# Kernel tuning notes

Measured on AMD Instinct MI355X. Metric: run time of the kernel, lower is better.

The kernel has to match this reference:

```python
import jax, jax.numpy as jnp
import numpy as np

T_TOTAL = 90  # t_total init arg (static decode length)


def _gru_cell(x, h, w_ih, w_hh, b_ih, b_hh):
    # PyTorch nn.GRUCell math
    gi = x @ w_ih.T + b_ih
    gh = h @ w_hh.T + b_hh
    i_r, i_z, i_n = jnp.split(gi, 3, axis=-1)
    h_r, h_z, h_n = jnp.split(gh, 3, axis=-1)
    r = jax.nn.sigmoid(i_r + h_r)
    z = jax.nn.sigmoid(i_z + h_z)
    n = jnp.tanh(i_n + r * h_n)
    return (1.0 - z) * n + z * h


def setup_inputs() -> dict:
    key = jax.random.key(0)
    T, B, NX, H, NZ = 90, 2048, 144, 128, 128
    M1, M2 = 300, 200
    ks = jax.random.split(key, 24)
    def p(k, shape):
        return jax.random.normal(k, shape, dtype=jnp.float32) * 0.05
    return {
        "x": jax.random.normal(ks[0], (T, B, NX), dtype=jnp.float32),
        # encoder GRUCell (nx -> H)
        "w_ih_e": p(ks[1], (3 * H, NX)), "w_hh_e": p(ks[2], (3 * H, H)),
        "b_ih_e": p(ks[3], (3 * H,)),   "b_hh_e": p(ks[4], (3 * H,)),
        # encoder MLP (tanh) H->300->200
        "W1e": p(ks[5], (M1, H)),  "b1e": p(ks[6], (M1,)),
        "W2e": p(ks[7], (M2, M1)), "b2e": p(ks[8], (M2,)),
        # latent heads 200->NZ
        "Wmu": p(ks[9], (NZ, M2)),  "bmu": p(ks[10], (NZ,)),
        "Wlv": p(ks[11], (NZ, M2)), "blv": p(ks[12], (NZ,)),
        # decoder GRUCell (nx+nz -> H)
        "w_ih_d": p(ks[13], (3 * H, NX + NZ)), "w_hh_d": p(ks[14], (3 * H, H)),
        "b_ih_d": p(ks[15], (3 * H,)),          "b_hh_d": p(ks[16], (3 * H,)),
        # decoder MLP (tanh) H->300->200 and output 200->nx
        "W1d": p(ks[17], (M1, H)),  "b1d": p(ks[18], (M1,)),
        "W2d": p(ks[19], (M2, M1)), "b2d": p(ks[20], (M2,)),
        "Wo": p(ks[21], (NX, M2)),  "bo": p(ks[22], (NX,)),
    }


def reference(x, w_ih_e, w_hh_e, b_ih_e, b_hh_e, W1e, b1e, W2e, b2e,
              Wmu, bmu, Wlv, blv, w_ih_d, w_hh_d, b_ih_d, b_hh_d,
              W1d, b1d, W2d, b2d, Wo, bo):
    B = x.shape[1]
    H = w_hh_e.shape[1]
    h0 = jnp.zeros((B, H), dtype=x.dtype)

    # ---- encode: GRU over time, take last hidden ----
    def enc_step(h, xt):
        return _gru_cell(xt, h, w_ih_e, w_hh_e, b_ih_e, b_hh_e), None
    h_x, _ = jax.lax.scan(enc_step, h0, x)  # (B, H)
    he = jnp.tanh(h_x @ W1e.T + b1e)
    he = jnp.tanh(he @ W2e.T + b2e)
    mu = he @ Wmu.T + bmu
    logvar = he @ Wlv.T + blv
    z = mu  # eval mode: z = mu (no reparameterization noise)

    def dec_step(carry, _):
        hd, xp = carry
        rnn_in = jnp.concatenate([xp, z], axis=1)  # (B, NX+NZ)
        hd = _gru_cell(rnn_in, hd, w_ih_d, w_hh_d, b_ih_d, b_hh_d)
        m = jnp.tanh(hd @ W1d.T + b1d)
        m = jnp.tanh(m @ W2d.T + b2d)
        xi = m @ Wo.T + bo
        return (hd, xi), xi

    _, x_rec = jax.lax.scan(dec_step, (h0, x[0]), None, length=T_TOTAL)
    return x_rec, mu, logvar
```

## Files before the change

### kernel.cpp

```cpp
#include <hip/hip_runtime.h>
#include <cstddef>

#define T_STEPS 90
#define BT      2048
#define NXV     144
#define HV      128
#define NZV     128
#define M1V     300
#define M2V     200
#define NB      16
#define NTH     512

typedef __attribute__((ext_vector_type(8))) _Float16 half8v;
typedef __attribute__((ext_vector_type(4))) float f32x4;

constexpr int MTa[12]   = {24,24,19,13, 8, 8,24,24,24,19,13, 9};
constexpr int MREAL[12] = {384,384,300,200,128,128,384,384,384,300,200,144};
constexpr int KREAL[12] = {144,128,128,300,200,200,144,128,128,128,300,200};
constexpr int RSW[12]   = {144,128,128,300,200,200,272,272,128,128,300,200};
constexpr int COW[12]   = {  0,  0,  0,  0,  0,  0,  0,144,  0,  0,  0,  0};
constexpr int P13[13]   = {0,120,240,335,465,521,577,697,817,937,1032,1162,1225};
constexpr int NFRAG = 1225;

__device__ __forceinline__ float fsig(float v)  { return 1.0f / (1.0f + __expf(-v)); }
__device__ __forceinline__ float ftanh(float v) { return 1.0f - 2.0f / (__expf(2.0f * v) + 1.0f); }

__global__ void __launch_bounds__(64)
prep_frags(const float* __restrict__ w_ih_e, const float* __restrict__ w_hh_e,
           const float* __restrict__ W1e,    const float* __restrict__ W2e,
           const float* __restrict__ Wmu,    const float* __restrict__ Wlv,
           const float* __restrict__ w_ih_d, const float* __restrict__ w_hh_d,
           const float* __restrict__ W1d,    const float* __restrict__ W2d,
           const float* __restrict__ Wo,
           const float* __restrict__ b_ih_e, const float* __restrict__ b_hh_e,
           const float* __restrict__ b1e,    const float* __restrict__ b2e,
           const float* __restrict__ bmu,    const float* __restrict__ blv,
           const float* __restrict__ b_ih_d, const float* __restrict__ b_hh_d,
           const float* __restrict__ b1d,    const float* __restrict__ b2d,
           const float* __restrict__ bo,
           _Float16* __restrict__ ws)
{
    int f = blockIdx.x;
    int g = 0;
    while (g < 11 && f >= P13[g + 1]) ++g;
    int fl = f - P13[g];
    int MT = MTa[g];
    int kt = fl / MT, mt = fl - kt * MT;

    const float* W; const float* bias;
    switch (g) {
        case 0:  W = w_ih_e; bias = b_ih_e; break;
        case 1:  W = w_hh_e; bias = b_hh_e; break;
        case 2:  W = W1e;    bias = b1e;    break;
        case 3:  W = W2e;    bias = b2e;    break;
        case 4:  W = Wmu;    bias = bmu;    break;
        case 5:  W = Wlv;    bias = blv;    break;
        case 6:  W = w_ih_d; bias = nullptr; break;
        case 7:  W = w_ih_d; bias = b_ih_d; break;
        case 8:  W = w_hh_d; bias = b_hh_d; break;
        case 9:  W = W1d;    bias = b1d;    break;
        case 10: W = W2d;    bias = b2d;    break;
        default: W = Wo;     bias = bo;     break;
    }
    int l = threadIdx.x;
    int m  = mt * 16 + (l & 15);
    int kb = kt * 32 + (l >> 4) * 8;
    _Float16* dst = ws + (size_t)f * 512 + (size_t)l * 8;
    #pragma unroll
    for (int j = 0; j < 8; ++j) {
        int k = kb + j;
        float val = 0.0f;
        if (m < MREAL[g]) {
            if (k < KREAL[g]) val = W[(size_t)m * RSW[g] + COW[g] + k];
            else if (k == KREAL[g] && bias) val = bias[m];
        }
        dst[j] = (_Float16)val;
    }
}

template<int MT, int KT, int NT, int RS>
__device__ __forceinline__ void gemm_reg(const half8v (&af)[KT * NT],
                                         const _Float16* __restrict__ Bt,
                                         int w, int l, f32x4 (&acc)[NT])
{
    const int bo_ = (l & 15) * RS + ((l >> 4) << 3);
    #pragma unroll
    for (int kt = 0; kt < KT; ++kt) {
        half8v bf = *(const half8v*)(Bt + bo_ + kt * 32);
        #pragma unroll
        for (int i = 0; i < NT; ++i)
            if (w + 8 * i < MT)
                acc[i] = __builtin_amdgcn_mfma_f32_16x16x32_f16(af[kt * NT + i], bf, acc[i], 0, 0, 0);
    }
}

template<int MT, int KT, int NT, int RS>
__device__ __forceinline__ void mlp_stream(const half8v* __restrict__ A,
                                           const _Float16* __restrict__ Bt,
                                           int w, int l, f32x4 (&acc)[NT])
{
    half8v af[NT * KT];
    #pragma unroll
    for (int i = 0; i < NT; ++i) {
        int mt = w + 8 * i;
        if (mt < MT) {
            #pragma unroll
            for (int kt = 0; kt < KT; ++kt)
                af[i * KT + kt] = A[(size_t)(kt * MT + mt) * 64 + l];
        }
    }
    const int bo_ = (l & 15) * RS + ((l >> 4) << 3);
    #pragma unroll
    for (int kt = 0; kt < KT; ++kt) {
        half8v bf = *(const half8v*)(Bt + bo_ + kt * 32);
        #pragma unroll
        for (int i = 0; i < NT; ++i) {
            int mt = w + 8 * i;
            if (mt < MT)
                acc[i] = __builtin_amdgcn_mfma_f32_16x16x32_f16(af[i * KT + kt], bf, acc[i], 0, 0, 0);
        }
    }
}

template<int MT, int KT, int NT, int RS>
__device__ __forceinline__ void mlp_lds(const _Float16* __restrict__ Alds,
                                        const _Float16* __restrict__ Bt,
                                        int w, int l, f32x4 (&acc)[NT])
{
    const int bo_ = (l & 15) * RS + ((l >> 4) << 3);
    #pragma unroll
    for (int kt = 0; kt < KT; ++kt) {
        half8v bf = *(const half8v*)(Bt + bo_ + kt * 32);
        #pragma unroll
        for (int i = 0; i < NT; ++i) {
            int mt = w + 8 * i;
            if (mt < MT) {
                half8v af = *(const half8v*)(Alds + ((size_t)(kt * MT + mt) * 64 + l) * 8);
                acc[i] = __builtin_amdgcn_mfma_f32_16x16x32_f16(af, bf, acc[i], 0, 0, 0);
            }
        }
    }
}

template<int MT, int NT, int RS>
__device__ __forceinline__ void write_tanhN(const f32x4 (&acc)[NT], int Mreal,
                                            _Float16* __restrict__ T, int w, int l)
{
    int b = l & 15, q4 = (l >> 4) << 2;
    #pragma unroll
    for (int i = 0; i < NT; ++i) {
        int mt = w + 8 * i;
        if (mt < MT) {
            #pragma unroll
            for (int r = 0; r < 4; ++r) {
                int m = mt * 16 + q4 + r;
                if (m < Mreal) T[b * RS + m] = (_Float16)ftanh(acc[i][r]);
            }
        }
    }
}

__global__ void __launch_bounds__(NTH, 2)
vae_mfma(const float* __restrict__ x, const half8v* __restrict__ wsv,
         float* __restrict__ out)
{
    __shared__ __align__(16) _Float16 xT [NB * 168];
    __shared__ __align__(16) _Float16 hT [NB * 168];
    __shared__ __align__(16) _Float16 m1T[NB * 328];
    __shared__ __align__(16) _Float16 m2T[NB * 232];
    __shared__ __align__(16) _Float16 g10L[130 * 512];

    const int tid = threadIdx.x;
    const int w = tid >> 6, l = tid & 63;
    const int bbase = blockIdx.x * NB;
    const size_t XREC_SZ = (size_t)T_STEPS * BT * NXV;
    const size_t MU_OFF = XREC_SZ;
    const size_t LV_OFF = XREC_SZ + (size_t)BT * NZV;
    const f32x4 z4 = {0.f, 0.f, 0.f, 0.f};

#define AHI(g) (wsv + (size_t)P13[g] * 64)

    auto load_x = [&](int t, float xr[5]) {
        #pragma unroll
        for (int u = 0; u < 5; ++u) {
            int i = u * NTH + tid;
            if (i < NB * NXV)
                xr[u] = __builtin_nontemporal_load(
                    &x[(size_t)t * (BT * NXV) + (size_t)(bbase + i / NXV) * NXV + (i % NXV)]);
        }
    };
    auto store_x = [&](const float xr[5]) {
        #pragma unroll
        for (int u = 0; u < 5; ++u) {
            int i = u * NTH + tid;
            if (i < NB * NXV) {
                int b2 = i / NXV, k = i - b2 * NXV;
                xT[b2 * 168 + k] = (_Float16)xr[u];
            }
        }
    };

    half8v gih[15], ghh[15];
    half8v w1df[15];
    auto load_gates = [&](const half8v* Gih, const half8v* Ghh) {
        #pragma unroll
        for (int kt = 0; kt < 5; ++kt) {
            #pragma unroll
            for (int j = 0; j < 3; ++j) {
                gih[kt * 3 + j] = Gih[(size_t)(kt * 24 + w + 8 * j) * 64 + l];
                ghh[kt * 3 + j] = Ghh[(size_t)(kt * 24 + w + 8 * j) * 64 + l];
            }
        }
    };

    float hreg[4] = {0.f, 0.f, 0.f, 0.f};
    auto gru_combine = [&](const f32x4 (&ai)[3], const f32x4 (&ah)[3]) {
        #pragma unroll
        for (int r = 0; r < 4; ++r) {
            float rr = fsig(ai[0][r] + ah[0][r]);
            float zz = fsig(ai[1][r] + ah[1][r]);
            float nn = ftanh(ai[2][r] + rr * ah[2][r]);
            hreg[r] = (1.f - zz) * nn + zz * hreg[r];
        }
    };
    auto write_h = [&]() {
        int jb = 16 * w + ((l >> 4) << 2), b = l & 15;
        #pragma unroll
        for (int r = 0; r < 4; ++r) hT[b * 168 + jb + r] = (_Float16)hreg[r];
    };

    for (int i = tid; i < NB * 168; i += NTH) { xT[i] = (_Float16)0.f; hT[i] = (_Float16)0.f; }
    for (int i = tid; i < NB * 328; i += NTH) m1T[i] = (_Float16)0.f;
    for (int i = tid; i < NB * 232; i += NTH) m2T[i] = (_Float16)0.f;
    for (int i = tid; i < 130 * 64; i += NTH)
        *(half8v*)(g10L + (size_t)i * 8) = AHI(10)[i];
    load_gates(AHI(0), AHI(1));
    float xr[5] = {0, 0, 0, 0, 0};
    load_x(0, xr);
    __syncthreads();
    if (tid < NB) {
        xT [tid * 168 + 144] = (_Float16)1.f;
        hT [tid * 168 + 128] = (_Float16)1.f;
        m1T[tid * 328 + 300] = (_Float16)1.f;
        m2T[tid * 232 + 200] = (_Float16)1.f;
    }
    store_x(xr);
    load_x(1, xr);
    __syncthreads();

    for (int t = 0; t < T_STEPS; ++t) {
        f32x4 ai[3] = {z4, z4, z4}, ah[3] = {z4, z4, z4};
        gemm_reg<24, 5, 3, 168>(gih, xT, w, l, ai);
        gemm_reg<24, 5, 3, 168>(ghh, hT, w, l, ah);
        gru_combine(ai, ah);
        __syncthreads();
        write_h();
        if (t + 1 < T_STEPS) {
            store_x(xr);
            if (t + 2 < T_STEPS) load_x(t + 2, xr);
        }
        __syncthreads();
    }

    {
        f32x4 a1[3] = {z4, z4, z4};
        mlp_stream<19, 5, 3, 168>(AHI(2), hT, w, l, a1);
        write_tanhN<19, 3, 328>(a1, M1V, m1T, w, l);
        __syncthreads();
        f32x4 a2[2] = {z4, z4};
        mlp_stream<13, 10, 2, 328>(AHI(3), m1T, w, l, a2);
        write_tanhN<13, 2, 232>(a2, M2V, m2T, w, l);
        __syncthreads();
        f32x4 am[1] = {z4}, av[1] = {z4};
        mlp_stream<8, 7, 1, 232>(AHI(4), m2T, w, l, am);
        mlp_stream<8, 7, 1, 232>(AHI(5), m2T, w, l, av);
        __syncthreads();
        int b = l & 15, q4 = (l >> 4) << 2;
        int m = w * 16 + q4;
        __builtin_nontemporal_store(am[0], (f32x4*)&out[MU_OFF + (size_t)(bbase + b) * NZV + m]);
        __builtin_nontemporal_store(av[0], (f32x4*)&out[LV_OFF + (size_t)(bbase + b) * NZV + m]);
        #pragma unroll
        for (int r = 0; r < 4; ++r)
            m1T[b * 328 + m + r] = (_Float16)am[0][r];
    }

    f32x4 gzr[3] = {z4, z4, z4};
    {
        for (int i = tid; i < NB * HV; i += NTH) {
            int b2 = i >> 7, j = i & 127;
            hT[b2 * 168 + j] = (_Float16)0.f;
        }
        if (tid < NB) m1T[tid * 328 + 128] = (_Float16)1.f;
        float xr0[5] = {0, 0, 0, 0, 0};
        load_x(0, xr0);
        store_x(xr0);
        __syncthreads();
        mlp_stream<24, 5, 3, 328>(AHI(7), m1T, w, l, gzr);
        load_gates(AHI(6), AHI(8));
        #pragma unroll
        for (int kt = 0; kt < 5; ++kt) {
            #pragma unroll
            for (int j = 0; j < 3; ++j)
                if (w + 8 * j < 19)
                    w1df[kt * 3 + j] = AHI(9)[(size_t)(kt * 19 + w + 8 * j) * 64 + l];
        }
        #pragma unroll
        for (int r = 0; r < 4; ++r) hreg[r] = 0.f;
    }
    __syncthreads();

    for (int t = 0; t < T_STEPS; ++t) {
        f32x4 ai[3], ah[3];
        #pragma unroll
        for (int i = 0; i < 3; ++i) { ai[i] = gzr[i]; ah[i] = z4; }
        gemm_reg<24, 5, 3, 168>(gih, xT, w, l, ai);
        gemm_reg<24, 5, 3, 168>(ghh, hT, w, l, ah);
        gru_combine(ai, ah);
        __syncthreads();
        write_h();
        __syncthreads();
        f32x4 a1[3] = {z4, z4, z4};
        gemm_reg<19, 5, 3, 168>(w1df, hT, w, l, a1);
        write_tanhN<19, 3, 328>(a1, M1V, m1T, w, l);
        __syncthreads();
        half8v wo_af[14];
        #pragma unroll
        for (int kt = 0; kt < 7; ++kt) {
            #pragma unroll
            for (int i = 0; i < 2; ++i)
                if (w + 8 * i < 9)
                    wo_af[kt * 2 + i] = AHI(11)[(size_t)(kt * 9 + w + 8 * i) * 64 + l];
        }
        f32x4 a2[2] = {z4, z4};
        mlp_lds<13, 10, 2, 328>(g10L, m1T, w, l, a2);
        write_tanhN<13, 2, 232>(a2, M2V, m2T, w, l);
        __syncthreads();
        f32x4 ao[2] = {z4, z4};
        gemm_reg<9, 7, 2, 232>(wo_af, m2T, w, l, ao);
        {
            int b = l & 15, q4 = (l >> 4) << 2;
            #pragma unroll
            for (int i2 = 0; i2 < 2; ++i2) {
                int mt = w + 8 * i2;
                if (mt < 9) {
                    int m = mt * 16 + q4;
                    __builtin_nontemporal_store(ao[i2],
                        (f32x4*)&out[(size_t)t * (BT * NXV) + (size_t)(bbase + b) * NXV + m]);
                    #pragma unroll
                    for (int r = 0; r < 4; ++r)
                        xT[b * 168 + m + r] = (_Float16)ao[i2][r];
                }
            }
        }
        __syncthreads();
    }
#undef AHI
}

extern "C" void kernel_launch(void* const* d_in, const int* in_sizes, int n_in,
                              void* d_out, int out_size, void* d_ws, size_t ws_size,
                              hipStream_t stream) {
    (void)in_sizes; (void)n_in; (void)out_size; (void)ws_size;
    const float* p[23];
    for (int i = 0; i < 23; ++i) p[i] = (const float*)d_in[i];
    _Float16* ws = (_Float16*)d_ws;

    prep_frags<<<dim3(NFRAG), dim3(64), 0, stream>>>(
        p[1], p[2], p[5], p[7], p[9], p[11], p[13], p[14], p[17], p[19], p[21],
        p[3], p[4], p[6], p[8], p[10], p[12], p[15], p[16], p[18], p[20], p[22],
        ws);

    vae_mfma<<<dim3(BT / NB), dim3(NTH), 0, stream>>>(
        p[0], (const half8v*)ws, (float*)d_out);
}
```

Baseline: 912.5 us.

## Move biases to register epilogues, double-buffer hidden state, split W2d between LDS and registers

Biases are no longer folded into the weight fragments as an extra K column. They are held in registers and added in the GRU combine and tanh epilogues, with vectorized half4 LDS writes. The hidden-state and input LDS tiles are double-buffered, which removes one __syncthreads per encoder and decoder step. The decoder's second MLP layer keeps the first six K-tiles in LDS and the last four in registers, shrinking the LDS footprint. Register pressure rises (w2df, wo14, bias arrays), and dropping the bias column can shorten some K loops.

```diff
diff --git a/kernel.cpp b/kernel.cpp
--- a/kernel.cpp
+++ b/kernel.cpp
@@ -12,6 +12,7 @@
 #define NTH     512
 
 typedef __attribute__((ext_vector_type(8))) _Float16 half8v;
+typedef __attribute__((ext_vector_type(4))) _Float16 half4v;
 typedef __attribute__((ext_vector_type(4))) float f32x4;
 
 constexpr int MTa[12]   = {24,24,19,13, 8, 8,24,24,24,19,13, 9};
@@ -32,12 +33,6 @@
            const float* __restrict__ w_ih_d, const float* __restrict__ w_hh_d,
            const float* __restrict__ W1d,    const float* __restrict__ W2d,
            const float* __restrict__ Wo,
-           const float* __restrict__ b_ih_e, const float* __restrict__ b_hh_e,
-           const float* __restrict__ b1e,    const float* __restrict__ b2e,
-           const float* __restrict__ bmu,    const float* __restrict__ blv,
-           const float* __restrict__ b_ih_d, const float* __restrict__ b_hh_d,
-           const float* __restrict__ b1d,    const float* __restrict__ b2d,
-           const float* __restrict__ bo,
            _Float16* __restrict__ ws)
 {
     int f = blockIdx.x;
@@ -46,21 +41,14 @@
     int fl = f - P13[g];
     int MT = MTa[g];
     int kt = fl / MT, mt = fl - kt * MT;
-
-    const float* W; const float* bias;
+    const float* W;
     switch (g) {
-        case 0:  W = w_ih_e; bias = b_ih_e; break;
-        case 1:  W = w_hh_e; bias = b_hh_e; break;
-        case 2:  W = W1e;    bias = b1e;    break;
-        case 3:  W = W2e;    bias = b2e;    break;
-        case 4:  W = Wmu;    bias = bmu;    break;
-        case 5:  W = Wlv;    bias = blv;    break;
-        case 6:  W = w_ih_d; bias = nullptr; break;
-        case 7:  W = w_ih_d; bias = b_ih_d; break;
-        case 8:  W = w_hh_d; bias = b_hh_d; break;
-        case 9:  W = W1d;    bias = b1d;    break;
-        case 10: W = W2d;    bias = b2d;    break;
-        default: W = Wo;     bias = bo;     break;
+        case 0:  W = w_ih_e; break;  case 1:  W = w_hh_e; break;
+        case 2:  W = W1e;    break;  case 3:  W = W2e;    break;
+        case 4:  W = Wmu;    break;  case 5:  W = Wlv;    break;
+        case 6:  W = w_ih_d; break;  case 7:  W = w_ih_d; break;
+        case 8:  W = w_hh_d; break;  case 9:  W = W1d;    break;
+        case 10: W = W2d;    break;  default: W = Wo;     break;
     }
     int l = threadIdx.x;
     int m  = mt * 16 + (l & 15);
@@ -69,17 +57,14 @@
     #pragma unroll
     for (int j = 0; j < 8; ++j) {
         int k = kb + j;
-        float val = 0.0f;
-        if (m < MREAL[g]) {
-            if (k < KREAL[g]) val = W[(size_t)m * RSW[g] + COW[g] + k];
-            else if (k == KREAL[g] && bias) val = bias[m];
-        }
+        float val = (m < MREAL[g] && k < KREAL[g])
+                  ? W[(size_t)m * RSW[g] + COW[g] + k] : 0.0f;
         dst[j] = (_Float16)val;
     }
 }
 
 template<int MT, int KT, int NT, int RS>
-__device__ __forceinline__ void gemm_reg(const half8v (&af)[KT * NT],
+__device__ __forceinline__ void gemm_reg(const half8v* af,
                                          const _Float16* __restrict__ Bt,
                                          int w, int l, f32x4 (&acc)[NT])
 {
@@ -114,36 +99,14 @@
     for (int kt = 0; kt < KT; ++kt) {
         half8v bf = *(const half8v*)(Bt + bo_ + kt * 32);
         #pragma unroll
-        for (int i = 0; i < NT; ++i) {
-            int mt = w + 8 * i;
-            if (mt < MT)
+        for (int i = 0; i < NT; ++i)
+            if (w + 8 * i < MT)
                 acc[i] = __builtin_amdgcn_mfma_f32_16x16x32_f16(af[i * KT + kt], bf, acc[i], 0, 0, 0);
-        }
-    }
-}
-
-template<int MT, int KT, int NT, int RS>
-__device__ __forceinline__ void mlp_lds(const _Float16* __restrict__ Alds,
-                                        const _Float16* __restrict__ Bt,
-                                        int w, int l, f32x4 (&acc)[NT])
-{
-    const int bo_ = (l & 15) * RS + ((l >> 4) << 3);
-    #pragma unroll
-    for (int kt = 0; kt < KT; ++kt) {
-        half8v bf = *(const half8v*)(Bt + bo_ + kt * 32);
-        #pragma unroll
-        for (int i = 0; i < NT; ++i) {
-            int mt = w + 8 * i;
-            if (mt < MT) {
-                half8v af = *(const half8v*)(Alds + ((size_t)(kt * MT + mt) * 64 + l) * 8);
-                acc[i] = __builtin_amdgcn_mfma_f32_16x16x32_f16(af, bf, acc[i], 0, 0, 0);
-            }
-        }
     }
 }
 
 template<int MT, int NT, int RS>
-__device__ __forceinline__ void write_tanhN(const f32x4 (&acc)[NT], int Mreal,
+__device__ __forceinline__ void write_tanhV(const f32x4 (&acc)[NT], const float* bias,
                                             _Float16* __restrict__ T, int w, int l)
 {
     int b = l & 15, q4 = (l >> 4) << 2;
@@ -151,27 +114,35 @@
     for (int i = 0; i < NT; ++i) {
         int mt = w + 8 * i;
         if (mt < MT) {
-            #pragma unroll
-            for (int r = 0; r < 4; ++r) {
-                int m = mt * 16 + q4 + r;
-                if (m < Mreal) T[b * RS + m] = (_Float16)ftanh(acc[i][r]);
-            }
+            half4v v;
+            #pragma unroll
+            for (int r = 0; r < 4; ++r) v[r] = (_Float16)ftanh(acc[i][r] + bias[i * 4 + r]);
+            *(half4v*)&T[b * RS + mt * 16 + q4] = v;
         }
     }
 }
 
 __global__ void __launch_bounds__(NTH, 2)
 vae_mfma(const float* __restrict__ x, const half8v* __restrict__ wsv,
+         const float* __restrict__ b_ih_e, const float* __restrict__ b_hh_e,
+         const float* __restrict__ b1e,    const float* __restrict__ b2e,
+         const float* __restrict__ bmu,    const float* __restrict__ blv,
+         const float* __restrict__ b_ih_d, const float* __restrict__ b_hh_d,
+         const float* __restrict__ b1d,    const float* __restrict__ b2d,
+         const float* __restrict__ bo,
          float* __restrict__ out)
 {
-    __shared__ __align__(16) _Float16 xT [NB * 168];
-    __shared__ __align__(16) _Float16 hT [NB * 168];
+    __shared__ __align__(16) _Float16 xT [2][NB * 168];
+    __shared__ __align__(16) _Float16 hT [2][NB * 168];
     __shared__ __align__(16) _Float16 m1T[NB * 328];
     __shared__ __align__(16) _Float16 m2T[NB * 232];
-    __shared__ __align__(16) _Float16 g10L[130 * 512];
+    __shared__ __align__(16) _Float16 g10L[78 * 512];
 
     const int tid = threadIdx.x;
     const int w = tid >> 6, l = tid & 63;
+    const int b_ = l & 15;
+    const int q4 = (l >> 4) << 2;
+    const int u  = w * 16 + q4;
     const int bbase = blockIdx.x * NB;
     const size_t XREC_SZ = (size_t)T_STEPS * BT * NXV;
     const size_t MU_OFF = XREC_SZ;
@@ -182,81 +153,101 @@
 
     auto load_x = [&](int t, float xr[5]) {
         #pragma unroll
-        for (int u = 0; u < 5; ++u) {
-            int i = u * NTH + tid;
+        for (int uu = 0; uu < 5; ++uu) {
+            int i = uu * NTH + tid;
             if (i < NB * NXV)
-                xr[u] = __builtin_nontemporal_load(
+                xr[uu] = __builtin_nontemporal_load(
                     &x[(size_t)t * (BT * NXV) + (size_t)(bbase + i / NXV) * NXV + (i % NXV)]);
         }
     };
-    auto store_x = [&](const float xr[5]) {
-        #pragma unroll
-        for (int u = 0; u < 5; ++u) {
-            int i = u * NTH + tid;
+    auto store_x = [&](_Float16* dst, const float xr[5]) {
+        #pragma unroll
+        for (int uu = 0; uu < 5; ++uu) {
+            int i = uu * NTH + tid;
             if (i < NB * NXV) {
                 int b2 = i / NXV, k = i - b2 * NXV;
-                xT[b2 * 168 + k] = (_Float16)xr[u];
-            }
-        }
-    };
-
-    half8v gih[15], ghh[15];
-    half8v w1df[15];
+                dst[b2 * 168 + k] = (_Float16)xr[uu];
+            }
+        }
+    };
+
+    half8v gih[15] = {}, ghh[15] = {};
     auto load_gates = [&](const half8v* Gih, const half8v* Ghh) {
         #pragma unroll
-        for (int kt = 0; kt < 5; ++kt) {
+        for (int kt = 0; kt < 5; ++kt)
             #pragma unroll
             for (int j = 0; j < 3; ++j) {
                 gih[kt * 3 + j] = Gih[(size_t)(kt * 24 + w + 8 * j) * 64 + l];
                 ghh[kt * 3 + j] = Ghh[(size_t)(kt * 24 + w + 8 * j) * 64 + l];
             }
-        }
     };
 
     float hreg[4] = {0.f, 0.f, 0.f, 0.f};
+    float gb[16];
     auto gru_combine = [&](const f32x4 (&ai)[3], const f32x4 (&ah)[3]) {
         #pragma unroll
         for (int r = 0; r < 4; ++r) {
-            float rr = fsig(ai[0][r] + ah[0][r]);
-            float zz = fsig(ai[1][r] + ah[1][r]);
-            float nn = ftanh(ai[2][r] + rr * ah[2][r]);
+            float rr = fsig(ai[0][r] + ah[0][r] + gb[r]);
+            float zz = fsig(ai[1][r] + ah[1][r] + gb[4 + r]);
+            float nn = ftanh(ai[2][r] + gb[8 + r] + rr * (ah[2][r] + gb[12 + r]));
             hreg[r] = (1.f - zz) * nn + zz * hreg[r];
         }
     };
-    auto write_h = [&]() {
-        int jb = 16 * w + ((l >> 4) << 2), b = l & 15;
-        #pragma unroll
-        for (int r = 0; r < 4; ++r) hT[b * 168 + jb + r] = (_Float16)hreg[r];
-    };
-
-    for (int i = tid; i < NB * 168; i += NTH) { xT[i] = (_Float16)0.f; hT[i] = (_Float16)0.f; }
+    auto write_h = [&](int p) {
+        half4v v;
+        #pragma unroll
+        for (int r = 0; r < 4; ++r) v[r] = (_Float16)hreg[r];
+        *(half4v*)&hT[p][b_ * 168 + u] = v;
+    };
+
+    float b1r[12], b2r[8];
+    auto load_mlp_bias = [&](const float* B1, const float* B2) {
+        #pragma unroll
+        for (int i = 0; i < 3; ++i)
+            #pragma unroll
+            for (int r = 0; r < 4; ++r) {
+                int m = (w + 8 * i) * 16 + q4 + r;
+                b1r[i * 4 + r] = B1[m < M1V ? m : M1V - 1];
+            }
+        #pragma unroll
+        for (int i = 0; i < 2; ++i)
+            #pragma unroll
+            for (int r = 0; r < 4; ++r) {
+                int m = (w + 8 * i) * 16 + q4 + r;
+                b2r[i * 4 + r] = B2[m < M2V ? m : M2V - 1];
+            }
+    };
+
+    for (int i = tid; i < 2 * NB * 168; i += NTH) { ((_Float16*)xT)[i] = (_Float16)0.f; ((_Float16*)hT)[i] = (_Float16)0.f; }
     for (int i = tid; i < NB * 328; i += NTH) m1T[i] = (_Float16)0.f;
     for (int i = tid; i < NB * 232; i += NTH) m2T[i] = (_Float16)0.f;
-    for (int i = tid; i < 130 * 64; i += NTH)
+    for (int i = tid; i < 78 * 64; i += NTH)
         *(half8v*)(g10L + (size_t)i * 8) = AHI(10)[i];
     load_gates(AHI(0), AHI(1));
+    #pragma unroll
+    for (int r = 0; r < 4; ++r) {
+        gb[r]      = b_ih_e[u + r]       + b_hh_e[u + r];
+        gb[4 + r]  = b_ih_e[128 + u + r] + b_hh_e[128 + u + r];
+        gb[8 + r]  = b_ih_e[256 + u + r];
+        gb[12 + r] = b_hh_e[256 + u + r];
+    }
+    load_mlp_bias(b1e, b2e);
     float xr[5] = {0, 0, 0, 0, 0};
     load_x(0, xr);
     __syncthreads();
-    if (tid < NB) {
-        xT [tid * 168 + 144] = (_Float16)1.f;
-        hT [tid * 168 + 128] = (_Float16)1.f;
-        m1T[tid * 328 + 300] = (_Float16)1.f;
-        m2T[tid * 232 + 200] = (_Float16)1.f;
-    }
-    store_x(xr);
+    store_x(xT[0], xr);
     load_x(1, xr);
     __syncthreads();
 
     for (int t = 0; t < T_STEPS; ++t) {
+        int p = t & 1;
         f32x4 ai[3] = {z4, z4, z4}, ah[3] = {z4, z4, z4};
-        gemm_reg<24, 5, 3, 168>(gih, xT, w, l, ai);
-        gemm_reg<24, 5, 3, 168>(ghh, hT, w, l, ah);
+        gemm_reg<24, 5, 3, 168>(gih, xT[p], w, l, ai);
+        gemm_reg<24, 5, 3, 168>(ghh, hT[p], w, l, ah);
         gru_combine(ai, ah);
-        __syncthreads();
-        write_h();
+        write_h(p ^ 1);
         if (t + 1 < T_STEPS) {
-            store_x(xr);
+            store_x(xT[p ^ 1], xr);
             if (t + 2 < T_STEPS) load_x(t + 2, xr);
         }
         __syncthreads();
@@ -264,92 +255,135 @@
 
     {
         f32x4 a1[3] = {z4, z4, z4};
-        mlp_stream<19, 5, 3, 168>(AHI(2), hT, w, l, a1);
-        write_tanhN<19, 3, 328>(a1, M1V, m1T, w, l);
+        mlp_stream<19, 5, 3, 168>(AHI(2), hT[0], w, l, a1);
+        write_tanhV<19, 3, 328>(a1, b1r, m1T, w, l);
         __syncthreads();
         f32x4 a2[2] = {z4, z4};
         mlp_stream<13, 10, 2, 328>(AHI(3), m1T, w, l, a2);
-        write_tanhN<13, 2, 232>(a2, M2V, m2T, w, l);
+        write_tanhV<13, 2, 232>(a2, b2r, m2T, w, l);
         __syncthreads();
         f32x4 am[1] = {z4}, av[1] = {z4};
         mlp_stream<8, 7, 1, 232>(AHI(4), m2T, w, l, am);
         mlp_stream<8, 7, 1, 232>(AHI(5), m2T, w, l, av);
-        __syncthreads();
-        int b = l & 15, q4 = (l >> 4) << 2;
-        int m = w * 16 + q4;
-        __builtin_nontemporal_store(am[0], (f32x4*)&out[MU_OFF + (size_t)(bbase + b) * NZV + m]);
-        __builtin_nontemporal_store(av[0], (f32x4*)&out[LV_OFF + (size_t)(bbase + b) * NZV + m]);
-        #pragma unroll
-        for (int r = 0; r < 4; ++r)
-            m1T[b * 328 + m + r] = (_Float16)am[0][r];
-    }
+        f32x4 vm, vv;
+        half4v zv;
+        #pragma unroll
+        for (int r = 0; r < 4; ++r) {
+            vm[r] = am[0][r] + bmu[u + r];
+            vv[r] = av[0][r] + blv[u + r];
+            zv[r] = (_Float16)vm[r];
+        }
+        __builtin_nontemporal_store(vm, (f32x4*)&out[MU_OFF + (size_t)(bbase + b_) * NZV + u]);
+        __builtin_nontemporal_store(vv, (f32x4*)&out[LV_OFF + (size_t)(bbase + b_) * NZV + u]);
+        *(half4v*)&m1T[b_ * 328 + u] = zv;
+    }
+    __syncthreads();
 
     f32x4 gzr[3] = {z4, z4, z4};
+    half8v w1df[15] = {}, w2df[8] = {}, wo14[14] = {};
     {
-        for (int i = tid; i < NB * HV; i += NTH) {
-            int b2 = i >> 7, j = i & 127;
-            hT[b2 * 168 + j] = (_Float16)0.f;
-        }
-        if (tid < NB) m1T[tid * 328 + 128] = (_Float16)1.f;
+        for (int i = tid; i < NB * 168; i += NTH) hT[0][i] = (_Float16)0.f;
         float xr0[5] = {0, 0, 0, 0, 0};
         load_x(0, xr0);
-        store_x(xr0);
-        __syncthreads();
+        store_x(xT[0], xr0);
         mlp_stream<24, 5, 3, 328>(AHI(7), m1T, w, l, gzr);
+        #pragma unroll
+        for (int j = 0; j < 3; ++j)
+            #pragma unroll
+            for (int r = 0; r < 4; ++r) gzr[j][r] += b_ih_d[u + 128 * j + r];
         load_gates(AHI(6), AHI(8));
         #pragma unroll
-        for (int kt = 0; kt < 5; ++kt) {
+        for (int kt = 0; kt < 5; ++kt)
             #pragma unroll
             for (int j = 0; j < 3; ++j)
                 if (w + 8 * j < 19)
                     w1df[kt * 3 + j] = AHI(9)[(size_t)(kt * 19 + w + 8 * j) * 64 + l];
-        }
-        #pragma unroll
-        for (int r = 0; r < 4; ++r) hreg[r] = 0.f;
-    }
-    __syncthreads();
-
-    for (int t = 0; t < T_STEPS; ++t) {
-        f32x4 ai[3], ah[3];
-        #pragma unroll
-        for (int i = 0; i < 3; ++i) { ai[i] = gzr[i]; ah[i] = z4; }
-        gemm_reg<24, 5, 3, 168>(gih, xT, w, l, ai);
-        gemm_reg<24, 5, 3, 168>(ghh, hT, w, l, ah);
-        gru_combine(ai, ah);
-        __syncthreads();
-        write_h();
-        __syncthreads();
-        f32x4 a1[3] = {z4, z4, z4};
-        gemm_reg<19, 5, 3, 168>(w1df, hT, w, l, a1);
-        write_tanhN<19, 3, 328>(a1, M1V, m1T, w, l);
-        __syncthreads();
-        half8v wo_af[14];
-        #pragma unroll
-        for (int kt = 0; kt < 7; ++kt) {
+        #pragma unroll
+        for (int kt = 0; kt < 4; ++kt)
+            #pragma unroll
+            for (int i = 0; i < 2; ++i)
+                if (w + 8 * i < 13)
+                    w2df[kt * 2 + i] = AHI(10)[(size_t)((6 + kt) * 13 + w + 8 * i) * 64 + l];
+        #pragma unroll
+        for (int kt = 0; kt < 7; ++kt)
             #pragma unroll
             for (int i = 0; i < 2; ++i)
                 if (w + 8 * i < 9)
-                    wo_af[kt * 2 + i] = AHI(11)[(size_t)(kt * 9 + w + 8 * i) * 64 + l];
-        }
+                    wo14[kt * 2 + i] = AHI(11)[(size_t)(kt * 9 + w + 8 * i) * 64 + l];
+        #pragma unroll
+        for (int r = 0; r < 4; ++r) {
+            gb[r]      = b_hh_d[u + r];
+            gb[4 + r]  = b_hh_d[128 + u + r];
+            gb[8 + r]  = 0.f;
+            gb[12 + r] = b_hh_d[256 + u + r];
+            hreg[r] = 0.f;
+        }
+        load_mlp_bias(b1d, b2d);
+    }
+    float bor[8];
+    #pragma unroll
+    for (int i = 0; i < 2; ++i)
+        #pragma unroll
+        for (int r = 0; r < 4; ++r) {
+            int m = (w + 8 * i) * 16 + q4 + r;
+            bor[i * 4 + r] = bo[m < NXV ? m : NXV - 1];
+        }
+    __syncthreads();
+
+    for (int t = 0; t < T_STEPS; ++t) {
+        int q = t & 1;
+        f32x4 ai[3], ah[3];
+        #pragma unroll
+        for (int i = 0; i < 3; ++i) { ai[i] = gzr[i]; ah[i] = z4; }
+        gemm_reg<24, 5, 3, 168>(gih, xT[0], w, l, ai);
+        gemm_reg<24, 5, 3, 168>(ghh, hT[q], w, l, ah);
+        gru_combine(ai, ah);
+        write_h(q ^ 1);
+        __syncthreads();
+        f32x4 a1[3] = {z4, z4, z4};
+        gemm_reg<19, 5, 3, 168>(w1df, hT[q ^ 1], w, l, a1);
+        write_tanhV<19, 3, 328>(a1, b1r, m1T, w, l);
+        __syncthreads();
         f32x4 a2[2] = {z4, z4};
-        mlp_lds<13, 10, 2, 328>(g10L, m1T, w, l, a2);
-        write_tanhN<13, 2, 232>(a2, M2V, m2T, w, l);
+        {
+            const int bo2 = b_ * 328 + ((l >> 4) << 3);
+            #pragma unroll
+            for (int kt = 0; kt < 6; ++kt) {
+                half8v bf = *(const half8v*)(m1T + bo2 + kt * 32);
+                #pragma unroll
+                for (int i = 0; i < 2; ++i)
+                    if (w + 8 * i < 13) {
+                        half8v af = *(const half8v*)(g10L + ((size_t)(kt * 13 + w + 8 * i) * 64 + l) * 8);
+                        a2[i] = __builtin_amdgcn_mfma_f32_16x16x32_f16(af, bf, a2[i], 0, 0, 0);
+                    }
+            }
+            #pragma unroll
+            for (int kt = 0; kt < 4; ++kt) {
+                half8v bf = *(const half8v*)(m1T + bo2 + (6 + kt) * 32);
+                #pragma unroll
+                for (int i = 0; i < 2; ++i)
+                    if (w + 8 * i < 13)
+                        a2[i] = __builtin_amdgcn_mfma_f32_16x16x32_f16(w2df[kt * 2 + i], bf, a2[i], 0, 0, 0);
+            }
+        }
+        write_tanhV<13, 2, 232>(a2, b2r, m2T, w, l);
         __syncthreads();
         f32x4 ao[2] = {z4, z4};
-        gemm_reg<9, 7, 2, 232>(wo_af, m2T, w, l, ao);
-        {
-            int b = l & 15, q4 = (l >> 4) << 2;
-            #pragma unroll
-            for (int i2 = 0; i2 < 2; ++i2) {
-                int mt = w + 8 * i2;
-                if (mt < 9) {
-                    int m = mt * 16 + q4;
-                    __builtin_nontemporal_store(ao[i2],
-                        (f32x4*)&out[(size_t)t * (BT * NXV) + (size_t)(bbase + b) * NXV + m]);
-                    #pragma unroll
-                    for (int r = 0; r < 4; ++r)
-                        xT[b * 168 + m + r] = (_Float16)ao[i2][r];
+        gemm_reg<9, 7, 2, 232>(wo14, m2T, w, l, ao);
+        #pragma unroll
+        for (int i2 = 0; i2 < 2; ++i2) {
+            int mt = w + 8 * i2;
+            if (mt < 9) {
+                f32x4 vo;
+                half4v vh;
+                #pragma unroll
+                for (int r = 0; r < 4; ++r) {
+                    vo[r] = ao[i2][r] + bor[i2 * 4 + r];
+                    vh[r] = (_Float16)vo[r];
                 }
+                __builtin_nontemporal_store(vo,
+                    (f32x4*)&out[(size_t)t * (BT * NXV) + (size_t)(bbase + b_) * NXV + mt * 16 + q4]);
+                *(half4v*)&xT[0][b_ * 168 + mt * 16 + q4] = vh;
             }
         }
         __syncthreads();
@@ -366,10 +400,15 @@
     _Float16* ws = (_Float16*)d_ws;
 
     prep_frags<<<dim3(NFRAG), dim3(64), 0, stream>>>(
-        p[1], p[2], p[5], p[7], p[9], p[11], p[13], p[14], p[17], p[19], p[21],
-        p[3], p[4], p[6], p[8], p[10], p[12], p[15], p[16], p[18], p[20], p[22],
-        ws);
+        p[1], p[2], p[5], p[7], p[9], p[11], p[13], p[14], p[17], p[19], p[21], ws);
 
     vae_mfma<<<dim3(BT / NB), dim3(NTH), 0, stream>>>(
-        p[0], (const half8v*)ws, (float*)d_out);
-}
+        p[0], (const half8v*)ws,
+        p[3], p[4],
+        p[6], p[8],
+        p[10], p[12],
+        p[15], p[16],
+        p[18], p[20],
+        p[22],
+        (float*)d_out);
+}
```

Result: slower. 1.130 ms (+23.8%).
